# Kernel tuning notes

Measured on AMD Instinct MI355X. Metric: run time of the kernel, lower is better.

The kernel has to match this reference:

```python
import jax, jax.numpy as jnp
import numpy as np

NUM_HEADS = 8
EPS = 1e-12  # F.normalize default eps


def setup_inputs() -> dict:
    key = jax.random.key(0)
    ks = jax.random.split(key, 6)
    dim = 64
    b, h, w = 1, 64, 64
    x = jax.random.normal(ks[0], (b, dim, h, w), dtype=jnp.float32)
    y = jax.random.normal(ks[1], (b, dim, h, w), dtype=jnp.float32)
    # 1x1 conv weights (kernel dims squeezed), kaiming-ish scale
    s = 1.0 / np.sqrt(dim)
    w_q = jax.random.normal(ks[2], (dim, dim), dtype=jnp.float32) * s
    w_kv = jax.random.normal(ks[3], (2 * dim, dim), dtype=jnp.float32) * s
    w_out = jax.random.normal(ks[4], (dim, dim), dtype=jnp.float32) * s
    temperature = jnp.ones((NUM_HEADS, 1, 1), dtype=jnp.float32)
    return {"x": x, "y": y, "w_q": w_q, "w_kv": w_kv, "w_out": w_out,
            "temperature": temperature}


def _l2norm(t):
    n = jnp.sqrt(jnp.sum(t * t, axis=-1, keepdims=True))
    return t / jnp.maximum(n, EPS)


def reference(x, y, w_q, w_kv, w_out, temperature):
    b, c, h, w = x.shape
    hd = c // NUM_HEADS  # per-head channel dim
    # 1x1 convs == channel matmuls
    q = jnp.einsum('oc,bchw->bohw', w_q, x)
    kv = jnp.einsum('oc,bchw->bohw', w_kv, y)
    k, v = jnp.split(kv, 2, axis=1)
    def to_heads(t):  # b (head c) h w -> b head (h w) c
        return t.reshape(b, NUM_HEADS, hd, h * w).transpose(0, 1, 3, 2)
    q, k, v = to_heads(q), to_heads(k), to_heads(v)
    q = _l2norm(q)
    k = _l2norm(k)
    # cosine-similarity logits scaled by learned per-head temperature
    attn = jnp.einsum('bhnc,bhmc->bhnm', q, k) * temperature[None]
    attn = jax.nn.softmax(attn, axis=-1)
    out = jnp.einsum('bhnm,bhmc->bhnc', attn, v)
    out = out.transpose(0, 1, 3, 2).reshape(b, c, h, w)
    return jnp.einsum('oc,bchw->bohw', w_out, out)
```

## Files before the change

kernel.cpp:

```cpp
#include <hip/hip_runtime.h>
#include <hip/hip_bf16.h>

#define DIM 64
#define N 4096
#define NH 8
#define HD 8
#define KPW 512
#define TKS 128

typedef __hip_bfloat16 bf16;
typedef __attribute__((ext_vector_type(8))) short short8;
typedef __attribute__((ext_vector_type(16))) float f32x16;
#define MFMA32 __builtin_amdgcn_mfma_f32_32x32x16_bf16

__device__ __forceinline__ float b2f(bf16 v) { return __bfloat162float(v); }

__device__ __forceinline__ bool is_bf16_mode(const void* temp) {
    return (((const unsigned*)temp)[0] & 0xFFFFu) != 0u;
}
__device__ __forceinline__ float ldany(const void* p, int i, bool isbf) {
    return isbf ? b2f(((const bf16*)p)[i]) : ((const float*)p)[i];
}
__device__ __forceinline__ unsigned pk(float a, float b) {
    union { __hip_bfloat162 h; unsigned u; } z;
    z.h = __float22bfloat162_rn(make_float2(a, b));
    return z.u;
}

__global__ __launch_bounds__(256) void proj_qkv(
    const void* __restrict__ x, const void* __restrict__ y,
    const void* __restrict__ w_q, const void* __restrict__ w_kv,
    const void* __restrict__ temp,
    ushort* __restrict__ qg, ushort* __restrict__ kg, ushort* __restrict__ vg)
{
    const bool isbf = is_bf16_mode(temp);
    const int mode = blockIdx.y;
    const int px = blockIdx.x * 32 + (threadIdx.x & 31);
    const int grp = threadIdx.x >> 5;
    const void* in = (mode == 0) ? x : y;
    const void* w  = (mode == 0) ? w_q : w_kv;
    const int woff = (mode == 2) ? DIM * DIM : 0;

    __shared__ float wl[DIM * DIM];
    for (int i = threadIdx.x; i < DIM * DIM; i += 256) {
        int o = i >> 6, c = i & 63;
        wl[c * DIM + o] = ldany(w, woff + i, isbf);
    }
    __syncthreads();

    float a[8];
#pragma unroll
    for (int o = 0; o < 8; o++) a[o] = 0.f;

#pragma unroll 8
    for (int c = 0; c < DIM; c++) {
        float xv = ldany(in, c * N + px, isbf);
        const float* wrow = &wl[c * DIM + grp * 8];
        float4 w0 = *(const float4*)&wrow[0];
        float4 w1 = *(const float4*)&wrow[4];
        a[0] = fmaf(w0.x, xv, a[0]); a[1] = fmaf(w0.y, xv, a[1]);
        a[2] = fmaf(w0.z, xv, a[2]); a[3] = fmaf(w0.w, xv, a[3]);
        a[4] = fmaf(w1.x, xv, a[4]); a[5] = fmaf(w1.y, xv, a[5]);
        a[6] = fmaf(w1.z, xv, a[6]); a[7] = fmaf(w1.w, xv, a[7]);
    }

    if (mode < 2) {
        float s = 0.f;
#pragma unroll
        for (int c = 0; c < 8; c++) s = fmaf(a[c], a[c], s);
        float inv = 1.0f / fmaxf(sqrtf(s), 1e-12f);
        if (mode == 0)
            inv *= ldany(temp, grp, isbf) * 1.44269504088896340736f;
#pragma unroll
        for (int c = 0; c < 8; c++) a[c] *= inv;
    }

    ushort* dst = (mode == 0) ? qg : (mode == 1 ? kg : vg);
    uint4 pkt;
    pkt.x = pk(a[0], a[1]); pkt.y = pk(a[2], a[3]);
    pkt.z = pk(a[4], a[5]); pkt.w = pk(a[6], a[7]);
    *(uint4*)(dst + ((size_t)grp * N + px) * 8) = pkt;
}

__global__ __launch_bounds__(512) void attn_mfma(
    const ushort* __restrict__ qg, const ushort* __restrict__ kg,
    const ushort* __restrict__ vg, float* __restrict__ og)
{
    const int h = blockIdx.y;
    const int qbase = blockIdx.x * 32;
    const int tid = threadIdx.x;
    const int wv = tid >> 6;
    const int lane = tid & 63;
    const int lr = lane & 31;
    const int g  = lane >> 5;

    __shared__ __align__(16) ushort vt[8 * 1320];
    __shared__ float pbuf[8 * 256];
    __shared__ float lbuf[8 * 32];
    __shared__ float linv[32];

    ushort* vtw = vt + wv * 1320;
    vtw[8 * 132 + lane]      = 0x3F80;
    vtw[8 * 132 + 64 + lane] = 0x3F80;
    vtw[9 * 132 + lane]      = 0;
    vtw[9 * 132 + 64 + lane] = 0;

    const ushort* qgh = qg + (size_t)h * N * 8;
    short8 qf = {0, 0, 0, 0, 0, 0, 0, 0};
    if (lane < 32) {
        uint4 t4 = *(const uint4*)(qgh + (size_t)(qbase + lr) * 8);
        unsigned* qu = (unsigned*)&qf;
        qu[0] = t4.x; qu[1] = t4.y; qu[2] = t4.z; qu[3] = t4.w;
    }

    const int swp = (lr & ~12) | ((lr & 4) << 1) | ((lr & 8) >> 1);
    const int rp = (lr <= 8) ? lr : 9;
    const ushort* vrp = vtw + rp * 132 + g * 8;

    const ushort* kgh = kg + (size_t)h * N * 8;
    const ushort* vgh = vg + (size_t)h * N * 8;

    f32x16 zz = {0,0,0,0,0,0,0,0,0,0,0,0,0,0,0,0};
    f32x16 o2 = {0,0,0,0,0,0,0,0,0,0,0,0,0,0,0,0};

    const int kb0 = wv * KPW;
    uint4 va = *(const uint4*)(vgh + (size_t)(kb0 + lane) * 8);
    uint4 vb = *(const uint4*)(vgh + (size_t)(kb0 + 64 + lane) * 8);
    uint4 kr0 = make_uint4(0,0,0,0), kr1 = make_uint4(0,0,0,0);
    uint4 kr2 = make_uint4(0,0,0,0), kr3 = make_uint4(0,0,0,0);
    if (lane < 32) {
        kr0 = *(const uint4*)(kgh + (size_t)(kb0 +  0 + swp) * 8);
        kr1 = *(const uint4*)(kgh + (size_t)(kb0 + 32 + swp) * 8);
        kr2 = *(const uint4*)(kgh + (size_t)(kb0 + 64 + swp) * 8);
        kr3 = *(const uint4*)(kgh + (size_t)(kb0 + 96 + swp) * 8);
    }

    for (int st = 0; st < KPW / TKS; st++) {
        {
            unsigned wa[4] = {va.x, va.y, va.z, va.w};
            unsigned wb[4] = {vb.x, vb.y, vb.z, vb.w};
#pragma unroll
            for (int c = 0; c < 4; c++) {
                vtw[(2 * c + 0) * 132 + lane]      = (ushort)(wa[c] & 0xFFFFu);
                vtw[(2 * c + 1) * 132 + lane]      = (ushort)(wa[c] >> 16);
                vtw[(2 * c + 0) * 132 + 64 + lane] = (ushort)(wb[c] & 0xFFFFu);
                vtw[(2 * c + 1) * 132 + 64 + lane] = (ushort)(wb[c] >> 16);
            }
        }

        const int kbn = wv * KPW + ((st < KPW / TKS - 1) ? (st + 1) : st) * TKS;
        uint4 van = *(const uint4*)(vgh + (size_t)(kbn + lane) * 8);
        uint4 vbn = *(const uint4*)(vgh + (size_t)(kbn + 64 + lane) * 8);
        uint4 krn0 = make_uint4(0,0,0,0), krn1 = make_uint4(0,0,0,0);
        uint4 krn2 = make_uint4(0,0,0,0), krn3 = make_uint4(0,0,0,0);

#pragma unroll
        for (int s = 0; s < 4; s++) {
            short8 kf;
            {
                uint4 ks = (s == 0) ? kr0 : (s == 1) ? kr1 : (s == 2) ? kr2 : kr3;
                unsigned* ku = (unsigned*)&kf;
                ku[0] = ks.x; ku[1] = ks.y; ku[2] = ks.z; ku[3] = ks.w;
            }
            if (lane < 32) {
                uint4 kn = *(const uint4*)(kgh + (size_t)(kbn + 32 * s + swp) * 8);
                if (s == 0) krn0 = kn; else if (s == 1) krn1 = kn;
                else if (s == 2) krn2 = kn; else krn3 = kn;
            }

            f32x16 d1 = MFMA32(kf, qf, zz, 0, 0, 0);

            short8 p0, p1;
            unsigned* p0u = (unsigned*)&p0;
            unsigned* p1u = (unsigned*)&p1;
#pragma unroll
            for (int w = 0; w < 4; w++) {
                p0u[w] = pk(__builtin_amdgcn_exp2f(d1[2 * w]),
                            __builtin_amdgcn_exp2f(d1[2 * w + 1]));
                p1u[w] = pk(__builtin_amdgcn_exp2f(d1[8 + 2 * w]),
                            __builtin_amdgcn_exp2f(d1[8 + 2 * w + 1]));
            }
#pragma unroll
            for (int t = 0; t < 2; t++) {
                const ushort* vpt = vrp + s * 32 + t * 16;
                short8 vf;
                uint2 vaa = *(const uint2*)(vpt + 0);
                uint2 vbb = *(const uint2*)(vpt + 4);
                unsigned* vu = (unsigned*)&vf;
                vu[0] = vaa.x; vu[1] = vaa.y; vu[2] = vbb.x; vu[3] = vbb.y;
                o2 = MFMA32(vf, t == 0 ? p0 : p1, o2, 0, 0, 0);
            }
        }
        va = van; vb = vbn;
        kr0 = krn0; kr1 = krn1; kr2 = krn2; kr3 = krn3;
    }

    *(float4*)&pbuf[wv * 256 + lr * 8 + g * 4] =
        make_float4(o2[0], o2[1], o2[2], o2[3]);
    if (g == 0) lbuf[wv * 32 + lr] = o2[4];
    __syncthreads();

    float sum = 0.f;
    if (tid < 256) {
        const int q = tid >> 3, ch = tid & 7;
#pragma unroll
        for (int w = 0; w < 8; w++) sum += pbuf[w * 256 + q * 8 + ch];
    } else if (tid < 288) {
        const int q = tid - 256;
        float L = 0.f;
#pragma unroll
        for (int w = 0; w < 8; w++) L += lbuf[w * 32 + q];
        linv[q] = 1.0f / L;
    }
    __syncthreads();

    if (tid < 256) {
        const int q = tid >> 3, ch = tid & 7;
        og[(size_t)(qbase + q) * DIM + h * 8 + ch] = sum * linv[q];
    }
}

__global__ __launch_bounds__(256) void out_proj(
    const float* __restrict__ og, const void* __restrict__ w_out,
    const void* __restrict__ temp, void* __restrict__ out)
{
    const bool isbf = is_bf16_mode(temp);
    const int px = blockIdx.x * 16 + (threadIdx.x & 15);
    const int grp = threadIdx.x >> 4;

    __shared__ float wl[DIM * DIM];
    for (int i = threadIdx.x; i < DIM * DIM; i += 256) {
        int o = i >> 6, c = i & 63;
        wl[c * DIM + o] = ldany(w_out, i, isbf);
    }
    __syncthreads();

    float a0 = 0.f, a1 = 0.f, a2 = 0.f, a3 = 0.f;
    const float4* og4 = (const float4*)(og + (size_t)px * DIM);
#pragma unroll 4
    for (int c4 = 0; c4 < DIM / 4; c4++) {
        float4 ov = og4[c4];
        float xs[4] = {ov.x, ov.y, ov.z, ov.w};
#pragma unroll
        for (int u = 0; u < 4; u++) {
            const float* wrow = &wl[(c4 * 4 + u) * DIM + grp * 4];
            float4 wv = *(const float4*)wrow;
            a0 = fmaf(wv.x, xs[u], a0); a1 = fmaf(wv.y, xs[u], a1);
            a2 = fmaf(wv.z, xs[u], a2); a3 = fmaf(wv.w, xs[u], a3);
        }
    }

    if (isbf) {
        bf16* ob = (bf16*)out;
        ob[(grp * 4 + 0) * N + px] = __float2bfloat16(a0);
        ob[(grp * 4 + 1) * N + px] = __float2bfloat16(a1);
        ob[(grp * 4 + 2) * N + px] = __float2bfloat16(a2);
        ob[(grp * 4 + 3) * N + px] = __float2bfloat16(a3);
    } else {
        float* of = (float*)out;
        of[(grp * 4 + 0) * N + px] = a0;
        of[(grp * 4 + 1) * N + px] = a1;
        of[(grp * 4 + 2) * N + px] = a2;
        of[(grp * 4 + 3) * N + px] = a3;
    }
}

extern "C" void kernel_launch(void* const* d_in, const int* in_sizes, int n_in,
                              void* d_out, int out_size, void* d_ws, size_t ws_size,
                              hipStream_t stream)
{
    const void* x     = d_in[0];
    const void* y     = d_in[1];
    const void* w_q   = d_in[2];
    const void* w_kv  = d_in[3];
    const void* w_out = d_in[4];
    const void* temp  = d_in[5];

    ushort* qg = (ushort*)d_ws;
    ushort* kg = qg + (size_t)NH * N * 8;
    ushort* vg = kg + (size_t)NH * N * 8;
    float*  og = (float*)(vg + (size_t)NH * N * 8);

    proj_qkv<<<dim3(N / 32, 3), 256, 0, stream>>>(x, y, w_q, w_kv, temp, qg, kg, vg);
    attn_mfma<<<dim3(N / 32, NH), 512, 0, stream>>>(qg, kg, vg, og);
    out_proj<<<dim3(N / 16), 256, 0, stream>>>(og, w_out, temp, d_out);
}
```

Measured before the change: 103.9 us.

## Cut attention kernel registers and LDS to raise occupancy, add MFMA priority

```diff
diff --git a/kernel.cpp b/kernel.cpp
--- a/kernel.cpp
+++ b/kernel.cpp
@@ -82,7 +82,7 @@
     *(uint4*)(dst + ((size_t)grp * N + px) * 8) = pkt;
 }
 
-__global__ __launch_bounds__(512) void attn_mfma(
+__global__ __launch_bounds__(512, 4) void attn_mfma(
     const ushort* __restrict__ qg, const ushort* __restrict__ kg,
     const ushort* __restrict__ vg, float* __restrict__ og)
 {
@@ -95,8 +95,6 @@
     const int g  = lane >> 5;
 
     __shared__ __align__(16) ushort vt[8 * 1320];
-    __shared__ float pbuf[8 * 256];
-    __shared__ float lbuf[8 * 32];
     __shared__ float linv[32];
 
     ushort* vtw = vt + wv * 1320;
@@ -126,13 +124,10 @@
     const int kb0 = wv * KPW;
     uint4 va = *(const uint4*)(vgh + (size_t)(kb0 + lane) * 8);
     uint4 vb = *(const uint4*)(vgh + (size_t)(kb0 + 64 + lane) * 8);
-    uint4 kr0 = make_uint4(0,0,0,0), kr1 = make_uint4(0,0,0,0);
-    uint4 kr2 = make_uint4(0,0,0,0), kr3 = make_uint4(0,0,0,0);
+    uint4 krA = make_uint4(0, 0, 0, 0), krB = make_uint4(0, 0, 0, 0);
     if (lane < 32) {
-        kr0 = *(const uint4*)(kgh + (size_t)(kb0 +  0 + swp) * 8);
-        kr1 = *(const uint4*)(kgh + (size_t)(kb0 + 32 + swp) * 8);
-        kr2 = *(const uint4*)(kgh + (size_t)(kb0 + 64 + swp) * 8);
-        kr3 = *(const uint4*)(kgh + (size_t)(kb0 + 96 + swp) * 8);
+        krA = *(const uint4*)(kgh + (size_t)(kb0 +  0 + swp) * 8);
+        krB = *(const uint4*)(kgh + (size_t)(kb0 + 32 + swp) * 8);
     }
 
     for (int st = 0; st < KPW / TKS; st++) {
@@ -151,23 +146,22 @@
         const int kbn = wv * KPW + ((st < KPW / TKS - 1) ? (st + 1) : st) * TKS;
         uint4 van = *(const uint4*)(vgh + (size_t)(kbn + lane) * 8);
         uint4 vbn = *(const uint4*)(vgh + (size_t)(kbn + 64 + lane) * 8);
-        uint4 krn0 = make_uint4(0,0,0,0), krn1 = make_uint4(0,0,0,0);
-        uint4 krn2 = make_uint4(0,0,0,0), krn3 = make_uint4(0,0,0,0);
 
 #pragma unroll
         for (int s = 0; s < 4; s++) {
+            const int j = st * 4 + s;
             short8 kf;
             {
-                uint4 ks = (s == 0) ? kr0 : (s == 1) ? kr1 : (s == 2) ? kr2 : kr3;
                 unsigned* ku = (unsigned*)&kf;
-                ku[0] = ks.x; ku[1] = ks.y; ku[2] = ks.z; ku[3] = ks.w;
-            }
+                ku[0] = krA.x; ku[1] = krA.y; ku[2] = krA.z; ku[3] = krA.w;
+            }
+            krA = krB;
             if (lane < 32) {
-                uint4 kn = *(const uint4*)(kgh + (size_t)(kbn + 32 * s + swp) * 8);
-                if (s == 0) krn0 = kn; else if (s == 1) krn1 = kn;
-                else if (s == 2) krn2 = kn; else krn3 = kn;
-            }
-
+                const int jn = (j + 2 <= 15) ? (j + 2) : 15;
+                krB = *(const uint4*)(kgh + (size_t)(kb0 + 32 * jn + swp) * 8);
+            }
+
+            __builtin_amdgcn_s_setprio(1);
             f32x16 d1 = MFMA32(kf, qf, zz, 0, 0, 0);
 
             short8 p0, p1;
@@ -190,26 +184,29 @@
                 vu[0] = vaa.x; vu[1] = vaa.y; vu[2] = vbb.x; vu[3] = vbb.y;
                 o2 = MFMA32(vf, t == 0 ? p0 : p1, o2, 0, 0, 0);
             }
+            __builtin_amdgcn_s_setprio(0);
         }
         va = van; vb = vbn;
-        kr0 = krn0; kr1 = krn1; kr2 = krn2; kr3 = krn3;
-    }
-
-    *(float4*)&pbuf[wv * 256 + lr * 8 + g * 4] =
+    }
+
+    float* combw = (float*)vt + wv * 660;
+    *(float4*)&combw[lr * 8 + g * 4] =
         make_float4(o2[0], o2[1], o2[2], o2[3]);
-    if (g == 0) lbuf[wv * 32 + lr] = o2[4];
+    if (g == 0) combw[256 + lr] = o2[4];
     __syncthreads();
 
     float sum = 0.f;
     if (tid < 256) {
         const int q = tid >> 3, ch = tid & 7;
-#pragma unroll
-        for (int w = 0; w < 8; w++) sum += pbuf[w * 256 + q * 8 + ch];
+        const float* vf = (const float*)vt;
+#pragma unroll
+        for (int w = 0; w < 8; w++) sum += vf[w * 660 + q * 8 + ch];
     } else if (tid < 288) {
         const int q = tid - 256;
+        const float* vf = (const float*)vt;
         float L = 0.f;
 #pragma unroll
-        for (int w = 0; w < 8; w++) L += lbuf[w * 32 + q];
+        for (int w = 0; w < 8; w++) L += vf[w * 660 + 256 + q];
         linv[q] = 1.0f / L;
     }
     __syncthreads();
```

Result: no change. 105.8 us (+1.8%).
